# Kernel optimization log

Hardware: AMD Instinct MI355X
Metric: run time of the kernel (lower is better)

Reference implementation:

```python
import jax, jax.numpy as jnp
import numpy as np

N_NODES = 50000
N_EDGES = 800000


def setup_inputs() -> dict:
    key = jax.random.key(0)
    ks = jax.random.split(key, 8)
    x = jax.random.normal(ks[0], (N_NODES, 256), dtype=jnp.float32)
    edge_index = jax.random.randint(ks[1], (2, N_EDGES), 0, N_NODES, dtype=jnp.int64)
    edge_weight = jax.random.uniform(ks[2], (N_EDGES,), dtype=jnp.float32)
    # Glorot-style weights for the 3 GCNConv layers: 256->128->64->32
    def glorot(k, fan_in, fan_out):
        s = jnp.sqrt(6.0 / (fan_in + fan_out))
        return jax.random.uniform(k, (fan_in, fan_out), dtype=jnp.float32, minval=-s, maxval=s)
    return {
        "x": x,
        "edge_index": edge_index,
        "edge_weight": edge_weight,
        "W1": glorot(ks[3], 256, 128), "b1": jnp.zeros((128,), jnp.float32),
        "W2": glorot(ks[4], 128, 64),  "b2": jnp.zeros((64,), jnp.float32),
        "W3": glorot(ks[5], 64, 32),   "b3": jnp.zeros((32,), jnp.float32),
    }


def _gcn_forward(x, row, col, ew, params):
    """Stacked GCNConv+ReLU (PyG semantics: add self loops, symmetric norm)."""
    n = x.shape[0]
    loop = jnp.arange(n, dtype=row.dtype)
    row_f = jnp.concatenate([row, loop])            # [E+N] sources
    col_f = jnp.concatenate([col, loop])            # [E+N] targets
    ew_f = jnp.concatenate([ew, jnp.ones((n,), ew.dtype)])
    deg = jax.ops.segment_sum(ew_f, col_f, num_segments=n)
    dinv = jnp.where(deg > 0, jax.lax.rsqrt(deg), 0.0)
    norm = dinv[row_f] * ew_f * dinv[col_f]         # [E+N]
    for W, b in params:
        h = x @ W                                   # [N, d_out] linear first (PyG order)
        msg = h[row_f] * norm[:, None]              # [E+N, d_out] gather + scale
        agg = jax.ops.segment_sum(msg, col_f, num_segments=n)  # scatter-add
        x = jax.nn.relu(agg + b)                    # fused bias + ReLU
    return x


def reference(x, edge_index, edge_weight, W1, b1, W2, b2, W3, b3):
    row, col = edge_index[0], edge_index[1]
    params = [(W1, b1), (W2, b2), (W3, b3)]
    return _gcn_forward(x, row, col, edge_weight, params)
```

## Files before the change

### kernel.cpp

```cpp
#include <hip/hip_runtime.h>
#include <hip/hip_fp16.h>


#define D0 256
#define D1 128
#define D2 64
#define D3 32

#define FIX_SCALE 16777216.0f
#define FIX_INV   (1.0f / 16777216.0f)

typedef _Float16 half8 __attribute__((ext_vector_type(8)));
typedef float floatx4 __attribute__((ext_vector_type(4)));

__device__ __forceinline__ void stage_slab(const float* __restrict__ X, int slab,
                                           _Float16 (*__restrict__ sA)[D0 + 8], int t) {
    const int row = t >> 4;
    const int c0 = (t & 15) * 16;
    const float* src = X + (size_t)(slab * 16 + row) * D0 + c0;
    float4 f0 = *(const float4*)(src + 0);
    float4 f1 = *(const float4*)(src + 4);
    float4 f2 = *(const float4*)(src + 8);
    float4 f3 = *(const float4*)(src + 12);
    half8 h0, h1;
    h0[0] = (_Float16)f0.x; h0[1] = (_Float16)f0.y;
    h0[2] = (_Float16)f0.z; h0[3] = (_Float16)f0.w;
    h0[4] = (_Float16)f1.x; h0[5] = (_Float16)f1.y;
    h0[6] = (_Float16)f1.z; h0[7] = (_Float16)f1.w;
    h1[0] = (_Float16)f2.x; h1[1] = (_Float16)f2.y;
    h1[2] = (_Float16)f2.z; h1[3] = (_Float16)f2.w;
    h1[4] = (_Float16)f3.x; h1[5] = (_Float16)f3.y;
    h1[6] = (_Float16)f3.z; h1[7] = (_Float16)f3.w;
    *(half8*)&sA[row][c0]     = h0;
    *(half8*)&sA[row][c0 + 8] = h1;
}

__global__ __launch_bounds__(256) void hist_gemm1_kernel(
        const float* __restrict__ x, const float* __restrict__ W1,
        _Float16* __restrict__ h1, int N,
        const int* __restrict__ ei, const float* __restrict__ ew,
        unsigned long long* __restrict__ pk, int* __restrict__ rank, int E,
        int gB) {
    __shared__ _Float16 sA[2][16][D0 + 8];
    const int b = blockIdx.x;
    if (b >= gB) {
        int e = (b - gB) * 256 + threadIdx.x;
        if (e < E) {
            int c = ei[E + e];
            unsigned int wfix = (unsigned int)(ew[e] * FIX_SCALE + 0.5f);
            unsigned long long old =
                atomicAdd(&pk[c], (1ULL << 32) | (unsigned long long)wfix);
            rank[e] = (int)(old >> 32);
        }
        return;
    }
    constexpr int NC = D0 / 32;
    const int tid = threadIdx.x;
    const int w = tid >> 6;
    const int lane = tid & 63;
    const int quad = lane >> 4;
    const int m = lane & 15;
    const int n0 = w * 32;

    half8 b0[NC], b1[NC];
#pragma unroll
    for (int c = 0; c < NC; ++c) {
#pragma unroll
        for (int j = 0; j < 8; ++j) {
            int k = c * 32 + quad * 8 + j;
            b0[c][j] = (_Float16)W1[(size_t)k * D1 + n0 + m];
            b1[c][j] = (_Float16)W1[(size_t)k * D1 + n0 + 16 + m];
        }
    }

    const int nslab = N >> 4;
    int slab = b;
    if (slab >= nslab) return;
    stage_slab(x, slab, sA[0], tid);
    __syncthreads();
    int buf = 0;
    while (true) {
        const int next = slab + gB;
        if (next < nslab) stage_slab(x, next, sA[buf ^ 1], tid);

        half8 a[NC];
#pragma unroll
        for (int c = 0; c < NC; ++c)
            a[c] = *(const half8*)&sA[buf][m][c * 32 + quad * 8];
        floatx4 acc0 = (floatx4){0.f, 0.f, 0.f, 0.f};
        floatx4 acc1 = (floatx4){0.f, 0.f, 0.f, 0.f};
#pragma unroll
        for (int c = 0; c < NC; ++c) {
            acc0 = __builtin_amdgcn_mfma_f32_16x16x32_f16(a[c], b0[c], acc0, 0, 0, 0);
            acc1 = __builtin_amdgcn_mfma_f32_16x16x32_f16(a[c], b1[c], acc1, 0, 0, 0);
        }

        const int r0 = slab * 16 + quad * 4;
#pragma unroll
        for (int r = 0; r < 4; ++r) {
            h1[(size_t)(r0 + r) * D1 + n0 + m]      = (_Float16)acc0[r];
            h1[(size_t)(r0 + r) * D1 + n0 + 16 + m] = (_Float16)acc1[r];
        }
        __syncthreads();
        if (next >= nslab) break;
        slab = next;
        buf ^= 1;
    }
}

__global__ __launch_bounds__(256) void scan_reduce(const unsigned long long* __restrict__ pk,
                                                   float* __restrict__ dinv,
                                                   int* __restrict__ cnt,
                                                   int* __restrict__ blockSum, int N) {
    __shared__ int s[256];
    const int t = threadIdx.x;
    const int i = blockIdx.x * 256 + t;
    int v = 0;
    if (i < N) {
        unsigned long long p = pk[i];
        float d = (float)(unsigned int)(p & 0xffffffffULL) * FIX_INV + 1.0f;
        dinv[i] = rsqrtf(d);
        v = (int)(p >> 32);
        cnt[i] = v;
    }
    s[t] = v;
    __syncthreads();
#pragma unroll
    for (int off = 128; off > 0; off >>= 1) {
        if (t < off) s[t] += s[t + off];
        __syncthreads();
    }
    if (t == 0) blockSum[blockIdx.x] = s[0];
}

__global__ __launch_bounds__(256) void scan_apply(const int* __restrict__ cnt,
                                                  const int* __restrict__ blockSum,
                                                  int* __restrict__ row_ptr, int N, int B) {
    __shared__ int bs[256];
    __shared__ int s[256];
    const int t = threadIdx.x;
    bs[t] = (t < B) ? blockSum[t] : 0;
    __syncthreads();
#pragma unroll
    for (int off = 1; off < 256; off <<= 1) {
        int u = (t >= off) ? bs[t - off] : 0;
        __syncthreads();
        bs[t] += u;
        __syncthreads();
    }
    const int myOff = (blockIdx.x > 0) ? bs[blockIdx.x - 1] : 0;
    const int i = blockIdx.x * 256 + t;
    const int v = (i < N) ? cnt[i] : 0;
    s[t] = v;
    __syncthreads();
#pragma unroll
    for (int off = 1; off < 256; off <<= 1) {
        int u = (t >= off) ? s[t - off] : 0;
        __syncthreads();
        s[t] += u;
        __syncthreads();
    }
    if (i < N) row_ptr[i] = s[t] - v + myOff;
    if (blockIdx.x == 0 && t == 0) row_ptr[N] = bs[B - 1];
}

__global__ void fill_kernel(const int* __restrict__ ei, const float* __restrict__ ew,
                            const float* __restrict__ dinv,
                            const int* __restrict__ row_ptr, const int* __restrict__ rank,
                            int2* __restrict__ pairs, int E) {
    int e = blockIdx.x * blockDim.x + threadIdx.x;
    if (e < E) {
        int r = ei[e];
        int c = ei[E + e];
        float w = dinv[r] * ew[e] * dinv[c];
        pairs[row_ptr[c] + rank[e]] = make_int2(r, __float_as_int(w));
    }
}

template <int DIN, int DOUT>
__global__ __launch_bounds__(256) void agg_gemm_kernel(
        const _Float16* __restrict__ H, const int* __restrict__ row_ptr,
        const int2* __restrict__ pairs, const float* __restrict__ dinv,
        const float* __restrict__ bias, const float* __restrict__ W,
        _Float16* __restrict__ Hout, int N) {
    constexpr int TPN = DIN / 8;
    constexpr int NPB = 256 / TPN;
    constexpr int NC  = DIN / 32;
    constexpr int S   = NPB / 16;
    constexpr int T   = DOUT / 16;
    static_assert(S * T == 4, "one tile per wave");
    __shared__ _Float16 sA[NPB][DIN + 8];

    const int tid = threadIdx.x;
    const int g = tid / TPN;
    const int sl = tid % TPN;
    const int node0 = blockIdx.x * NPB;
    const int node = node0 + g;
    const bool valid = node < N;

    const int w = tid >> 6;
    const int lane = tid & 63;
    const int q = lane >> 4;
    const int m = lane & 15;
    const int s = w & (S - 1);
    const int t = w / S;
    half8 bf[NC];
#pragma unroll
    for (int c = 0; c < NC; ++c) {
#pragma unroll
        for (int j = 0; j < 8; ++j)
            bf[c][j] = (_Float16)W[(size_t)(c * 32 + q * 8 + j) * DOUT + t * 16 + m];
    }

    float acc[8];
#pragma unroll
    for (int j = 0; j < 8; ++j) acc[j] = 0.0f;

    int beg = 0, end = 0;
    float di = 0.f;
    half8 uself = (half8){0,0,0,0,0,0,0,0};
    float bb[8];
    if (valid) {
        beg = row_ptr[node];
        end = row_ptr[node + 1];
        di = dinv[node];
        uself = *(const half8*)&H[(size_t)node * DIN + sl * 8];
        *(float4*)&bb[0] = *(const float4*)&bias[sl * 8];
        *(float4*)&bb[4] = *(const float4*)&bias[sl * 8 + 4];
    }

    if (end > beg) {
        const int last = end - 1;
        int2 p0 = pairs[beg];
        int2 p1 = pairs[min(beg + 1, last)];
        int2 p2 = pairs[min(beg + 2, last)];
        int2 p3 = pairs[min(beg + 3, last)];
        int2 p4 = pairs[min(beg + 4, last)];
        half8 u0 = *(const half8*)&H[(size_t)p0.x * DIN + sl * 8];
        half8 u1 = *(const half8*)&H[(size_t)p1.x * DIN + sl * 8];
        half8 u2 = *(const half8*)&H[(size_t)p2.x * DIN + sl * 8];
        half8 u3 = *(const half8*)&H[(size_t)p3.x * DIN + sl * 8];
        for (int k = beg; k < end; ++k) {
            int2 p5 = pairs[min(k + 5, last)];
            half8 u4 = *(const half8*)&H[(size_t)p4.x * DIN + sl * 8];
            float wv = __int_as_float(p0.y);
#pragma unroll
            for (int j = 0; j < 8; ++j) acc[j] = fmaf(wv, (float)u0[j], acc[j]);
            p0 = p1; p1 = p2; p2 = p3; p3 = p4; p4 = p5;
            u0 = u1; u1 = u2; u2 = u3; u3 = u4;
        }
    }

    if (valid) {
        float d2 = di * di;
#pragma unroll
        for (int j = 0; j < 8; ++j) acc[j] = fmaf(d2, (float)uself[j], acc[j]);
        half8 o;
#pragma unroll
        for (int j = 0; j < 8; ++j) o[j] = (_Float16)fmaxf(acc[j] + bb[j], 0.f);
        *(half8*)&sA[g][sl * 8] = o;
    }
    __syncthreads();

    half8 a[NC];
#pragma unroll
    for (int c = 0; c < NC; ++c)
        a[c] = *(const half8*)&sA[s * 16 + m][c * 32 + q * 8];
    floatx4 o4 = (floatx4){0.f, 0.f, 0.f, 0.f};
#pragma unroll
    for (int c = 0; c < NC; ++c)
        o4 = __builtin_amdgcn_mfma_f32_16x16x32_f16(a[c], bf[c], o4, 0, 0, 0);
#pragma unroll
    for (int r = 0; r < 4; ++r) {
        const int nr = node0 + s * 16 + q * 4 + r;
        if (nr < N) Hout[(size_t)nr * DOUT + t * 16 + m] = (_Float16)o4[r];
    }
}

__global__ __launch_bounds__(256) void agg2_split_kernel(
        const _Float16* __restrict__ H, const int* __restrict__ row_ptr,
        const int2* __restrict__ pairs, const float* __restrict__ dinv,
        const float* __restrict__ bias, const float* __restrict__ W,
        _Float16* __restrict__ Hout, int N) {
    __shared__ float pacc[16][64];
    __shared__ _Float16 sA[16][D2 + 8];
    const int tid = threadIdx.x;
    const int grp = tid >> 4;
    const int sub = (tid >> 3) & 1;
    const int sl  = tid & 7;
    const int node0 = blockIdx.x * 16;
    const int node = node0 + grp;
    const bool valid = node < N;

    float acc[8];
#pragma unroll
    for (int j = 0; j < 8; ++j) acc[j] = 0.0f;

    int beg = 0, end = 0;
    if (valid) { beg = row_ptr[node]; end = row_ptr[node + 1]; }

    const int kb = beg + sub;
    if (end > kb) {
        const int last = end - 1;
        int2 p0 = pairs[min(kb,     last)];
        int2 p1 = pairs[min(kb + 2, last)];
        int2 p2 = pairs[min(kb + 4, last)];
        int2 p3 = pairs[min(kb + 6, last)];
        int2 p4 = pairs[min(kb + 8, last)];
        half8 u0 = *(const half8*)&H[(size_t)p0.x * D2 + sl * 8];
        half8 u1 = *(const half8*)&H[(size_t)p1.x * D2 + sl * 8];
        half8 u2 = *(const half8*)&H[(size_t)p2.x * D2 + sl * 8];
        half8 u3 = *(const half8*)&H[(size_t)p3.x * D2 + sl * 8];
        for (int k = kb; k < end; k += 2) {
            int2 p5 = pairs[min(k + 10, last)];
            half8 u4 = *(const half8*)&H[(size_t)p4.x * D2 + sl * 8];
            float wv = __int_as_float(p0.y);
#pragma unroll
            for (int j = 0; j < 8; ++j) acc[j] = fmaf(wv, (float)u0[j], acc[j]);
            p0 = p1; p1 = p2; p2 = p3; p3 = p4; p4 = p5;
            u0 = u1; u1 = u2; u2 = u3; u3 = u4;
        }
    }
    if (valid && sub == 1) {
        *(float4*)&pacc[grp][sl * 8]     = make_float4(acc[0], acc[1], acc[2], acc[3]);
        *(float4*)&pacc[grp][sl * 8 + 4] = make_float4(acc[4], acc[5], acc[6], acc[7]);
    }
    __syncthreads();
    if (valid && sub == 0) {
        const float4 q0 = *(const float4*)&pacc[grp][sl * 8];
        const float4 q1 = *(const float4*)&pacc[grp][sl * 8 + 4];
        acc[0] += q0.x; acc[1] += q0.y; acc[2] += q0.z; acc[3] += q0.w;
        acc[4] += q1.x; acc[5] += q1.y; acc[6] += q1.z; acc[7] += q1.w;
        const float di = dinv[node];
        const float d2 = di * di;
        const half8 uself = *(const half8*)&H[(size_t)node * D2 + sl * 8];
#pragma unroll
        for (int j = 0; j < 8; ++j) acc[j] = fmaf(d2, (float)uself[j], acc[j]);
        float bb[8];
        *(float4*)&bb[0] = *(const float4*)&bias[sl * 8];
        *(float4*)&bb[4] = *(const float4*)&bias[sl * 8 + 4];
        half8 o;
#pragma unroll
        for (int j = 0; j < 8; ++j) o[j] = (_Float16)fmaxf(acc[j] + bb[j], 0.f);
        *(half8*)&sA[grp][sl * 8] = o;
    }
    __syncthreads();

    const int w = tid >> 6;
    const int lane = tid & 63;
    const int q = lane >> 4;
    const int m = lane & 15;
    if (w < 2) {
        half8 bf[2], a[2];
#pragma unroll
        for (int c = 0; c < 2; ++c) {
#pragma unroll
            for (int j = 0; j < 8; ++j)
                bf[c][j] = (_Float16)W[(size_t)(c * 32 + q * 8 + j) * D3 + w * 16 + m];
            a[c] = *(const half8*)&sA[m][c * 32 + q * 8];
        }
        floatx4 o4 = (floatx4){0.f, 0.f, 0.f, 0.f};
        o4 = __builtin_amdgcn_mfma_f32_16x16x32_f16(a[0], bf[0], o4, 0, 0, 0);
        o4 = __builtin_amdgcn_mfma_f32_16x16x32_f16(a[1], bf[1], o4, 0, 0, 0);
#pragma unroll
        for (int r = 0; r < 4; ++r) {
            const int nr = node0 + q * 4 + r;
            if (nr < N) Hout[(size_t)nr * D3 + w * 16 + m] = (_Float16)o4[r];
        }
    }
}

__global__ __launch_bounds__(256) void agg3_split_kernel(
        const _Float16* __restrict__ H, const int* __restrict__ row_ptr,
        const int2* __restrict__ pairs, const float* __restrict__ dinv,
        const float* __restrict__ bias, float* __restrict__ out, int N) {
    __shared__ float pacc[16][3][32];
    const int tid = threadIdx.x;
    const int grp = tid >> 4;
    const int sub = (tid >> 2) & 3;
    const int sl  = tid & 3;
    const int node = blockIdx.x * 16 + grp;
    const bool valid = node < N;

    float acc[8];
#pragma unroll
    for (int j = 0; j < 8; ++j) acc[j] = 0.0f;

    int beg = 0, end = 0;
    if (valid) { beg = row_ptr[node]; end = row_ptr[node + 1]; }

    const int kb = beg + sub;
    if (end > kb) {
        const int last = end - 1;
        int2 p0 = pairs[min(kb,      last)];
        int2 p1 = pairs[min(kb + 4,  last)];
        int2 p2 = pairs[min(kb + 8,  last)];
        int2 p3 = pairs[min(kb + 12, last)];
        int2 p4 = pairs[min(kb + 16, last)];
        half8 u0 = *(const half8*)&H[(size_t)p0.x * D3 + sl * 8];
        half8 u1 = *(const half8*)&H[(size_t)p1.x * D3 + sl * 8];
        half8 u2 = *(const half8*)&H[(size_t)p2.x * D3 + sl * 8];
        half8 u3 = *(const half8*)&H[(size_t)p3.x * D3 + sl * 8];
        for (int k = kb; k < end; k += 4) {
            int2 p5 = pairs[min(k + 20, last)];
            half8 u4 = *(const half8*)&H[(size_t)p4.x * D3 + sl * 8];
            float w = __int_as_float(p0.y);
#pragma unroll
            for (int j = 0; j < 8; ++j) acc[j] = fmaf(w, (float)u0[j], acc[j]);
            p0 = p1; p1 = p2; p2 = p3; p3 = p4; p4 = p5;
            u0 = u1; u1 = u2; u2 = u3; u3 = u4;
        }
    }
    if (valid && sub > 0) {
        *(float4*)&pacc[grp][sub - 1][sl * 8]     = make_float4(acc[0], acc[1], acc[2], acc[3]);
        *(float4*)&pacc[grp][sub - 1][sl * 8 + 4] = make_float4(acc[4], acc[5], acc[6], acc[7]);
    }
    __syncthreads();
    if (valid && sub == 0) {
#pragma unroll
        for (int s = 0; s < 3; ++s) {
            const float4 q0 = *(const float4*)&pacc[grp][s][sl * 8];
            const float4 q1 = *(const float4*)&pacc[grp][s][sl * 8 + 4];
            acc[0] += q0.x; acc[1] += q0.y; acc[2] += q0.z; acc[3] += q0.w;
            acc[4] += q1.x; acc[5] += q1.y; acc[6] += q1.z; acc[7] += q1.w;
        }
        const float di = dinv[node];
        const float d2 = di * di;
        const half8 uself = *(const half8*)&H[(size_t)node * D3 + sl * 8];
#pragma unroll
        for (int j = 0; j < 8; ++j) acc[j] = fmaf(d2, (float)uself[j], acc[j]);
        float bb[8];
        *(float4*)&bb[0] = *(const float4*)&bias[sl * 8];
        *(float4*)&bb[4] = *(const float4*)&bias[sl * 8 + 4];
#pragma unroll
        for (int j = 0; j < 8; ++j) acc[j] = fmaxf(acc[j] + bb[j], 0.f);
        float* dst = &out[(size_t)node * D3 + sl * 8];
        *(float4*)&dst[0] = make_float4(acc[0], acc[1], acc[2], acc[3]);
        *(float4*)&dst[4] = make_float4(acc[4], acc[5], acc[6], acc[7]);
    }
}

extern "C" void kernel_launch(void* const* d_in, const int* in_sizes, int n_in,
                              void* d_out, int out_size, void* d_ws, size_t ws_size,
                              hipStream_t stream) {
    const float* x   = (const float*)d_in[0];
    const int* ei    = (const int*)d_in[1];
    const float* ew  = (const float*)d_in[2];
    const float* W1  = (const float*)d_in[3];
    const float* b1  = (const float*)d_in[4];
    const float* W2  = (const float*)d_in[5];
    const float* b2  = (const float*)d_in[6];
    const float* W3  = (const float*)d_in[7];
    const float* b3  = (const float*)d_in[8];
    float* out = (float*)d_out;

    const int N = in_sizes[0] / D0;
    const int E = in_sizes[2];
    (void)n_in; (void)out_size; (void)ws_size;

    char* ws = (char*)d_ws;
    size_t off = 0;
    auto carve = [&](size_t bytes) -> void* {
        void* p = (void*)(ws + off);
        off += (bytes + 255) & ~(size_t)255;
        return p;
    };
    unsigned long long* pk = (unsigned long long*)carve((size_t)N * 8);
    float* dinv    = (float*)carve((size_t)N * 4);
    int*   cnt     = (int*)carve((size_t)N * 4);
    int*   row_ptr = (int*)carve((size_t)(N + 1) * 4);
    int*   rank    = (int*)carve((size_t)E * 4);
    int*   bsum    = (int*)carve(256 * 4);
    int2*  pairs   = (int2*)carve((size_t)E * 8);
    _Float16* bufH = (_Float16*)carve((size_t)N * D1 * 2);
    _Float16* bufO = (_Float16*)carve((size_t)N * D1 * 2);

    _Float16* h1 = bufH;
    _Float16* h2 = bufO;
    _Float16* h3 = bufH;

    const int eb = (E + 255) / 256;
    const int scanB = (N + 255) / 256;
    const int gB = 768;

    hipMemsetAsync(pk, 0, (size_t)N * 8, stream);
    hist_gemm1_kernel<<<gB + eb, 256, 0, stream>>>(
        x, W1, h1, N, ei, ew, pk, rank, E, gB);

    scan_reduce<<<scanB, 256, 0, stream>>>(pk, dinv, cnt, bsum, N);
    scan_apply<<<scanB, 256, 0, stream>>>(cnt, bsum, row_ptr, N, scanB);

    fill_kernel<<<eb, 256, 0, stream>>>(ei, ew, dinv, row_ptr, rank, pairs, E);

    agg_gemm_kernel<D1, D2><<<(N + 15) / 16, 256, 0, stream>>>(
        h1, row_ptr, pairs, dinv, b1, W2, h2, N);

    agg2_split_kernel<<<(N + 15) / 16, 256, 0, stream>>>(
        h2, row_ptr, pairs, dinv, b2, W3, h3, N);

    agg3_split_kernel<<<(N + 15) / 16, 256, 0, stream>>>(
        h3, row_ptr, pairs, dinv, b3, out, N);
}
```

Baseline: 243.0 us.

## Fuse two-pass scan into one kernel with grid-wide atomic barrier

Merges the scan_reduce and scan_apply kernels into a single kernel. Blocks publish their partial sums and spin on a global atomic counter until every block has arrived, then compute the prefix offsets. This removes one launch and the intermediate count array. It also raises the number of GEMM blocks in the first fused kernel. The spin barrier relies on all 196 blocks being co-resident, which holds on this GPU but is not guaranteed in general. The counter is zeroed by extending the existing memset.

```diff
diff --git a/kernel.cpp b/kernel.cpp
--- a/kernel.cpp
+++ b/kernel.cpp
@@ -108,11 +108,12 @@
     }
 }
 
-__global__ __launch_bounds__(256) void scan_reduce(const unsigned long long* __restrict__ pk,
-                                                   float* __restrict__ dinv,
-                                                   int* __restrict__ cnt,
-                                                   int* __restrict__ blockSum, int N) {
+__global__ __launch_bounds__(256) void scan_fused(
+        const unsigned long long* __restrict__ pk,
+        float* __restrict__ dinv, int* __restrict__ row_ptr,
+        int* __restrict__ bsum, int* __restrict__ done, int N, int B) {
     __shared__ int s[256];
+    __shared__ int bs[256];
     const int t = threadIdx.x;
     const int i = blockIdx.x * 256 + t;
     int v = 0;
@@ -121,25 +122,26 @@
         float d = (float)(unsigned int)(p & 0xffffffffULL) * FIX_INV + 1.0f;
         dinv[i] = rsqrtf(d);
         v = (int)(p >> 32);
-        cnt[i] = v;
     }
     s[t] = v;
     __syncthreads();
 #pragma unroll
-    for (int off = 128; off > 0; off >>= 1) {
-        if (t < off) s[t] += s[t + off];
+    for (int off = 1; off < 256; off <<= 1) {
+        int u = (t >= off) ? s[t - off] : 0;
         __syncthreads();
-    }
-    if (t == 0) blockSum[blockIdx.x] = s[0];
-}
-
-__global__ __launch_bounds__(256) void scan_apply(const int* __restrict__ cnt,
-                                                  const int* __restrict__ blockSum,
-                                                  int* __restrict__ row_ptr, int N, int B) {
-    __shared__ int bs[256];
-    __shared__ int s[256];
-    const int t = threadIdx.x;
-    bs[t] = (t < B) ? blockSum[t] : 0;
+        s[t] += u;
+        __syncthreads();
+    }
+    if (t == 0) {
+        bsum[blockIdx.x] = s[255];
+        __threadfence();
+        __hip_atomic_fetch_add(done, 1, __ATOMIC_RELEASE, __HIP_MEMORY_SCOPE_AGENT);
+        while (__hip_atomic_load(done, __ATOMIC_ACQUIRE, __HIP_MEMORY_SCOPE_AGENT) < B) {
+            __builtin_amdgcn_s_sleep(1);
+        }
+    }
+    __syncthreads();
+    bs[t] = (t < B) ? bsum[t] : 0;
     __syncthreads();
 #pragma unroll
     for (int off = 1; off < 256; off <<= 1) {
@@ -149,17 +151,6 @@
         __syncthreads();
     }
     const int myOff = (blockIdx.x > 0) ? bs[blockIdx.x - 1] : 0;
-    const int i = blockIdx.x * 256 + t;
-    const int v = (i < N) ? cnt[i] : 0;
-    s[t] = v;
-    __syncthreads();
-#pragma unroll
-    for (int off = 1; off < 256; off <<= 1) {
-        int u = (t >= off) ? s[t - off] : 0;
-        __syncthreads();
-        s[t] += u;
-        __syncthreads();
-    }
     if (i < N) row_ptr[i] = s[t] - v + myOff;
     if (blockIdx.x == 0 && t == 0) row_ptr[N] = bs[B - 1];
 }
@@ -465,9 +456,10 @@
         off += (bytes + 255) & ~(size_t)255;
         return p;
     };
+    const size_t pkBytes = ((size_t)N * 8 + 255) & ~(size_t)255;
     unsigned long long* pk = (unsigned long long*)carve((size_t)N * 8);
+    int*   done    = (int*)carve(256);
     float* dinv    = (float*)carve((size_t)N * 4);
-    int*   cnt     = (int*)carve((size_t)N * 4);
     int*   row_ptr = (int*)carve((size_t)(N + 1) * 4);
     int*   rank    = (int*)carve((size_t)E * 4);
     int*   bsum    = (int*)carve(256 * 4);
@@ -481,14 +473,14 @@
 
     const int eb = (E + 255) / 256;
     const int scanB = (N + 255) / 256;
-    const int gB = 768;
-
-    hipMemsetAsync(pk, 0, (size_t)N * 8, stream);
+    const int gB = 1280;
+
+    hipMemsetAsync(pk, 0, pkBytes + 256, stream);
+
     hist_gemm1_kernel<<<gB + eb, 256, 0, stream>>>(
         x, W1, h1, N, ei, ew, pk, rank, E, gB);
 
-    scan_reduce<<<scanB, 256, 0, stream>>>(pk, dinv, cnt, bsum, N);
-    scan_apply<<<scanB, 256, 0, stream>>>(cnt, bsum, row_ptr, N, scanB);
+    scan_fused<<<scanB, 256, 0, stream>>>(pk, dinv, row_ptr, bsum, done, N, scanB);
 
     fill_kernel<<<eb, 256, 0, stream>>>(ei, ew, dinv, row_ptr, rank, pairs, E);
 
```

After: 250.1 us. 1.03x slower.
